# Kernel optimization log

Measured on AMD Instinct MI355X. Metric: run time of the kernel, lower is better.

Reference implementation:

```python
import jax, jax.numpy as jnp
import numpy as np

B, H, W, F, D = 8, 126, 126, 64, 32
ITERS, NIT = 3, 20
RHO, NU, DT, FRC = 1.0, 0.1, 0.1, 1.0
DX = 2.0 / (B + 1)
DY = 2.0 / (H + 1)
DX2, DY2 = DX * DX, DY * DY
DEN = 2.0 * (DX2 + DY2)


def _b_term(du_dx, dv_dy, du_dy, dv_dx):
    return RHO * ((du_dx + dv_dy) / DT - du_dx**2 - 2.0 * du_dy * dv_dx - dv_dy**2)


def build_b(u, v):
    b = jnp.zeros_like(u)
    # interior
    b = b.at[:, 1:-1, 1:-1].set(_b_term(
        (u[:, 1:-1, 2:] - u[:, 1:-1, :-2]) / (2 * DX),
        (v[:, 2:, 1:-1] - v[:, :-2, 1:-1]) / (2 * DY),
        (u[:, 2:, 1:-1] - u[:, :-2, 1:-1]) / (2 * DY),
        (v[:, 1:-1, 2:] - v[:, 1:-1, :-2]) / (2 * DX)))
    # periodic wrap, last column
    b = b.at[:, 1:-1, -1].set(_b_term(
        (u[:, 1:-1, 0] - u[:, 1:-1, -2]) / (2 * DX),
        (v[:, 2:, -1] - v[:, :-2, -1]) / (2 * DY),
        (u[:, 2:, -1] - u[:, :-2, -1]) / (2 * DY),
        (v[:, 1:-1, 0] - v[:, 1:-1, -2]) / (2 * DX)))
    # periodic wrap, first column
    b = b.at[:, 1:-1, 0].set(_b_term(
        (u[:, 1:-1, 1] - u[:, 1:-1, -1]) / (2 * DX),
        (v[:, 2:, 0] - v[:, :-2, 0]) / (2 * DY),
        (u[:, 2:, 0] - u[:, :-2, 0]) / (2 * DY),
        (v[:, 1:-1, 1] - v[:, 1:-1, -1]) / (2 * DX)))
    return b


def pressure_poisson(p, b):
    c = DX2 * DY2 / DEN

    def step(p, _):
        pn = p
        p = p.at[:, 1:-1, 1:-1].set(
            ((pn[:, 1:-1, 2:] + pn[:, 1:-1, :-2]) * DY2 + (pn[:, 2:, 1:-1] + pn[:, :-2, 1:-1]) * DX2) / DEN
            - c * b[:, 1:-1, 1:-1])
        p = p.at[:, 1:-1, -1].set(
            ((pn[:, 1:-1, 0] + pn[:, 1:-1, -2]) * DY2 + (pn[:, 2:, -1] + pn[:, :-2, -1]) * DX2) / DEN
            - c * b[:, 1:-1, -1])
        p = p.at[:, 1:-1, 0].set(
            ((pn[:, 1:-1, 1] + pn[:, 1:-1, -1]) * DY2 + (pn[:, 2:, 0] + pn[:, :-2, 0]) * DX2) / DEN
            - c * b[:, 1:-1, 0])
        # Neumann-style row boundaries (copy from updated p, as in torch code)
        p = p.at[:, -1].set(p[:, -2])
        p = p.at[:, 0].set(p[:, 1])
        return p, None

    p, _ = jax.lax.scan(step, p, None, length=NIT)
    return p


def velocity_step(u, v, p):
    un, vn = u, v
    uc = un[:, 1:-1, 1:-1]
    vc = vn[:, 1:-1, 1:-1]
    u_i = (uc - uc * DT / DX * (uc - un[:, 1:-1, :-2]) - vc * DT / DY * (uc - un[:, :-2, 1:-1])
           - DT / (2 * RHO * DX) * (p[:, 1:-1, 2:] - p[:, 1:-1, :-2])
           + NU * (DT / DX2 * (un[:, 1:-1, 2:] - 2 * uc + un[:, 1:-1, :-2])
                   + DT / DY2 * (un[:, 2:, 1:-1] - 2 * uc + un[:, :-2, 1:-1]))
           + FRC * DT)
    v_i = (vc - uc * DT / DX * (vc - vn[:, 1:-1, :-2]) - vc * DT / DY * (vc - vn[:, :-2, 1:-1])
           - DT / (2 * RHO * DY) * (p[:, 2:, 1:-1] - p[:, :-2, 1:-1])
           + NU * (DT / DX2 * (vn[:, 1:-1, 2:] - 2 * vc + vn[:, 1:-1, :-2])
                   + DT / DY2 * (vn[:, 2:, 1:-1] - 2 * vc + vn[:, :-2, 1:-1])))
    ue = un[:, 1:-1, -1]
    ve = vn[:, 1:-1, -1]
    u_e = (ue - ue * DT / DX * (ue - un[:, 1:-1, -2]) - ve * DT / DY * (ue - un[:, :-2, -1])
           - DT / (2 * RHO * DX) * (p[:, 1:-1, 0] - p[:, 1:-1, -2])
           + NU * (DT / DX2 * (un[:, 1:-1, 0] - 2 * ue + un[:, 1:-1, -2])
                   + DT / DY2 * (un[:, 2:, -1] - 2 * ue + un[:, :-2, -1]))
           + FRC * DT)
    v_e = (ve - ue * DT / DX * (ve - vn[:, 1:-1, -2]) - ve * DT / DY * (ve - vn[:, :-2, -1])
           - DT / (2 * RHO * DY) * (p[:, 2:, -1] - p[:, :-2, -1])
           + NU * (DT / DX2 * (vn[:, 1:-1, 0] - 2 * ve + vn[:, 1:-1, -2])
                   + DT / DY2 * (vn[:, 2:, -1] - 2 * ve + vn[:, :-2, -1])))
    u0c = un[:, 1:-1, 0]
    v0c = vn[:, 1:-1, 0]
    u_0 = (u0c - u0c * DT / DX * (u0c - un[:, 1:-1, -1]) - v0c * DT / DY * (u0c - un[:, :-2, 0])
           - DT / (2 * RHO * DX) * (p[:, 1:-1, 1] - p[:, 1:-1, -1])
           + NU * (DT / DX2 * (un[:, 1:-1, 1] - 2 * u0c + un[:, 1:-1, -1])
                   + DT / DY2 * (un[:, 2:, 0] - 2 * u0c + un[:, :-2, 0]))
           + FRC * DT)
    v_0 = (v0c - u0c * DT / DX * (v0c - vn[:, 1:-1, -1]) - v0c * DT / DY * (v0c - vn[:, :-2, 0])
           - DT / (2 * RHO * DY) * (p[:, 2:, 0] - p[:, :-2, 0])
           + NU * (DT / DX2 * (vn[:, 1:-1, 1] - 2 * v0c + vn[:, 1:-1, -1])
                   + DT / DY2 * (vn[:, 2:, 0] - 2 * v0c + vn[:, :-2, 0])))
    u = un.at[:, 1:-1, 1:-1].set(u_i).at[:, 1:-1, -1].set(u_e).at[:, 1:-1, 0].set(u_0)
    v = vn.at[:, 1:-1, 1:-1].set(v_i).at[:, 1:-1, -1].set(v_e).at[:, 1:-1, 0].set(v_0)
    u = u.at[:, 0].set(0.0).at[:, -1].set(0.0)
    v = v.at[:, 0].set(0.0).at[:, -1].set(0.0)
    return u, v


def setup_inputs() -> dict:
    key = jax.random.key(0)
    ks = jax.random.split(key, 5)
    x = jax.random.normal(ks[0], (B, H, W, F), jnp.float32) * 0.05
    u0 = jax.random.normal(ks[1], (B, H + 2, W + 2, D), jnp.float32) * 0.05
    v0 = jax.random.normal(ks[2], (B, H + 2, W + 2, D), jnp.float32) * 0.05
    w = jax.random.normal(ks[3], (D, F), jnp.float32) / np.float32(np.sqrt(F))
    b_lin = jax.random.normal(ks[4], (D,), jnp.float32) * 0.01
    return {"x": x, "u0": u0, "v0": v0, "w": w, "b_lin": b_lin}


def reference(x, u0, v0, w, b_lin):
    # pad spatial dims by 1 then linear preprocess: (B,H+2,W+2,F) -> (B,H+2,W+2,D)
    p = jnp.pad(x, ((0, 0), (1, 1), (1, 1), (0, 0)))
    p = jnp.einsum('bhwf,df->bhwd', p, w) + b_lin
    u, v = u0, v0
    for _ in range(ITERS):
        b = build_b(u, v)
        p = pressure_poisson(p, b)
        u, v = velocity_step(u, v, p)
    return p[:, -1, :, :]  # (B, W+2, D)
```

## Files before the change

kernel.cpp:

```cpp
#include <hip/hip_runtime.h>

#define NITER 20
#define OUTER 3

constexpr double DXd  = 2.0 / 9.0;
constexpr double DYd  = 2.0 / 127.0;
constexpr double DX2d = DXd * DXd;
constexpr double DY2d = DYd * DYd;
constexpr double DENd = 2.0 * (DX2d + DY2d);

constexpr float K1     = (float)(DY2d / DENd);
constexpr float K2     = (float)(DX2d / DENd);
constexpr float CC     = (float)(DX2d * DY2d / DENd);
constexpr float INV2DX = (float)(1.0 / (2.0 * DXd));
constexpr float INV2DY = (float)(1.0 / (2.0 * DYd));
constexpr float INVDT  = (float)(1.0 / 0.1);
constexpr float DTDX   = (float)(0.1 / DXd);
constexpr float DTDY   = (float)(0.1 / DYd);
constexpr float PGX    = (float)(0.1 / (2.0 * 1.0 * DXd));
constexpr float PGY    = (float)(0.1 / (2.0 * 1.0 * DYd));
constexpr float A1     = (float)(0.1 / DX2d);
constexpr float A2     = (float)(0.1 / DY2d);
constexpr float NUf    = 0.1f;
constexpr float FDT    = 0.1f;

__device__ __forceinline__ float bperm(int srcByte, float v) {
    return __int_as_float(__builtin_amdgcn_ds_bpermute(srcByte, __float_as_int(v)));
}

__global__ __launch_bounds__(256) void einsum_kernel(
    const float* __restrict__ x, const float* __restrict__ w,
    const float* __restrict__ bl, float* __restrict__ p0)
{
    int id = blockIdx.x * 256 + threadIdx.x;
    int c = id & 127, r = (id >> 7) & 127, b = id >> 14;
    float acc[32];
#pragma unroll
    for (int d = 0; d < 32; ++d) acc[d] = bl[d];
    if (r >= 1 && r <= 126 && c >= 1 && c <= 126) {
        const float* xp = x + (((size_t)(b * 126 + (r - 1))) * 126 + (c - 1)) * 64;
#pragma unroll
        for (int f = 0; f < 64; f += 4) {
            float4 xv = *(const float4*)(xp + f);
#pragma unroll
            for (int d = 0; d < 32; ++d) {
                acc[d] += xv.x * w[d * 64 + f] + xv.y * w[d * 64 + f + 1]
                        + xv.z * w[d * 64 + f + 2] + xv.w * w[d * 64 + f + 3];
            }
        }
    }
    float* op = p0 + ((size_t)b * 32) * 16384 + r * 128 + c;
#pragma unroll
    for (int d = 0; d < 32; ++d) op[(size_t)d * 16384] = acc[d];
}

__global__ __launch_bounds__(1024, 4) void sim_kernel(
    const float* __restrict__ u0, const float* __restrict__ v0,
    const float* __restrict__ p0ws, const float* __restrict__ x,
    const float* __restrict__ w, const float* __restrict__ bl,
    float* __restrict__ out, int use_ws)
{
    __shared__ float S[32][4][128];

    const int tid = threadIdx.x;
    const int tx = tid & 31, ty = tid >> 5;
    const int c0 = tx << 2, r0 = ty << 2;
    const int lane = tid & 63;
    const int srcL = (((lane & 32) | ((lane + 31) & 31)) << 2);
    const int srcR = (((lane & 32) | ((lane + 1) & 31)) << 2);
    const int bb = blockIdx.x & 7;
    const int d  = blockIdx.x >> 3;
    const int tyN = (ty > 0) ? ty - 1 : 0;
    const int tyS = (ty < 31) ? ty + 1 : 31;

    float pC[4][4], uC[4][4], vC[4][4], cb[4][4];

#pragma unroll
    for (int r = 0; r < 4; ++r) {
        const size_t base = ((size_t)((bb * 128 + (r0 + r)) * 128 + c0)) * 32 + d;
#pragma unroll
        for (int c = 0; c < 4; ++c) {
            uC[r][c] = u0[base + (size_t)c * 32];
            vC[r][c] = v0[base + (size_t)c * 32];
        }
    }

    if (use_ws) {
        const float* pp = p0ws + ((size_t)(bb * 32 + d)) * 16384;
#pragma unroll
        for (int r = 0; r < 4; ++r) {
            float4 t = *(const float4*)(pp + (r0 + r) * 128 + c0);
            pC[r][0] = t.x; pC[r][1] = t.y; pC[r][2] = t.z; pC[r][3] = t.w;
        }
    } else {
        const float blv = bl[d];
#pragma unroll
        for (int r = 0; r < 4; ++r) {
            const int gr = r0 + r;
#pragma unroll
            for (int c = 0; c < 4; ++c) {
                const int gc = c0 + c;
                float acc = blv;
                if (gr >= 1 && gr <= 126 && gc >= 1 && gc <= 126) {
                    const float* xp = x + (((size_t)(bb * 126 + (gr - 1))) * 126 + (gc - 1)) * 64;
                    for (int f = 0; f < 64; f += 4) {
                        float4 xv = *(const float4*)(xp + f);
                        acc += xv.x * w[d * 64 + f] + xv.y * w[d * 64 + f + 1]
                             + xv.z * w[d * 64 + f + 2] + xv.w * w[d * 64 + f + 3];
                    }
                }
                pC[r][c] = acc;
            }
        }
    }

    *(float4*)&S[ty][0][c0] = make_float4(uC[0][0], uC[0][1], uC[0][2], uC[0][3]);
    *(float4*)&S[ty][1][c0] = make_float4(uC[3][0], uC[3][1], uC[3][2], uC[3][3]);
    *(float4*)&S[ty][2][c0] = make_float4(vC[0][0], vC[0][1], vC[0][2], vC[0][3]);
    *(float4*)&S[ty][3][c0] = make_float4(vC[3][0], vC[3][1], vC[3][2], vC[3][3]);
    __syncthreads();

    for (int outer = 0; outer < OUTER; ++outer) {
        float4 uN4 = *(const float4*)&S[tyN][1][c0];
        float4 uS4 = *(const float4*)&S[tyS][0][c0];
        float4 vN4 = *(const float4*)&S[tyN][3][c0];
        float4 vS4 = *(const float4*)&S[tyS][2][c0];
        float uNh[4] = {uN4.x, uN4.y, uN4.z, uN4.w};
        float uSh[4] = {uS4.x, uS4.y, uS4.z, uS4.w};
        float vNh[4] = {vN4.x, vN4.y, vN4.z, vN4.w};
        float vSh[4] = {vS4.x, vS4.y, vS4.z, vS4.w};

#pragma unroll
        for (int r = 0; r < 4; ++r) {
            float uWh = bperm(srcL, uC[r][3]);
            float uEh = bperm(srcR, uC[r][0]);
            float vWh = bperm(srcL, vC[r][3]);
            float vEh = bperm(srcR, vC[r][0]);
#pragma unroll
            for (int c = 0; c < 4; ++c) {
                float uE = (c < 3) ? uC[r][c + 1] : uEh;
                float uW = (c > 0) ? uC[r][c - 1] : uWh;
                float vE = (c < 3) ? vC[r][c + 1] : vEh;
                float vW = (c > 0) ? vC[r][c - 1] : vWh;
                float uN = (r > 0) ? uC[r - 1][c] : uNh[c];
                float uS_ = (r < 3) ? uC[r + 1][c] : uSh[c];
                float vN = (r > 0) ? vC[r - 1][c] : vNh[c];
                float vS_ = (r < 3) ? vC[r + 1][c] : vSh[c];
                float dudx = (uE - uW) * INV2DX;
                float dvdy = (vS_ - vN) * INV2DY;
                float dudy = (uS_ - uN) * INV2DY;
                float dvdx = (vE - vW) * INV2DX;
                float bt = (dudx + dvdy) * INVDT - dudx * dudx
                         - 2.0f * dudy * dvdx - dvdy * dvdy;
                cb[r][c] = CC * bt;
            }
        }
        __syncthreads();
        *(float4*)&S[ty][0][c0] = make_float4(pC[0][0], pC[0][1], pC[0][2], pC[0][3]);
        *(float4*)&S[ty][1][c0] = make_float4(pC[3][0], pC[3][1], pC[3][2], pC[3][3]);
        __syncthreads();

        for (int it = 0; it < NITER; ++it) {
            const int rb = (it & 1) << 1;
            const int wb = rb ^ 2;
            float4 t4 = *(const float4*)&S[tyN][rb + 1][c0];
            float4 b4 = *(const float4*)&S[tyS][rb + 0][c0];
            float nrow[4] = {t4.x, t4.y, t4.z, t4.w};
            float shalo[4] = {b4.x, b4.y, b4.z, b4.w};
            float pWh[4], pEh[4];
#pragma unroll
            for (int r = 0; r < 4; ++r) {
                pWh[r] = bperm(srcL, pC[r][3]);
                pEh[r] = bperm(srcR, pC[r][0]);
            }
#pragma unroll
            for (int r = 0; r < 4; ++r) {
                float old0[4];
#pragma unroll
                for (int c = 0; c < 4; ++c) old0[c] = pC[r][c];
#pragma unroll
                for (int c = 0; c < 4; ++c) {
                    float E = (c < 3) ? old0[c + 1] : pEh[r];
                    float W = (c > 0) ? old0[c - 1] : pWh[r];
                    float N = nrow[c];
                    float Sv = (r < 3) ? pC[r + 1][c] : shalo[c];
                    pC[r][c] = (E + W) * K1 + (N + Sv) * K2 - cb[r][c];
                }
#pragma unroll
                for (int c = 0; c < 4; ++c) nrow[c] = old0[c];
            }
            if (ty == 0) {
#pragma unroll
                for (int c = 0; c < 4; ++c) pC[0][c] = pC[1][c];
            }
            if (ty == 31) {
#pragma unroll
                for (int c = 0; c < 4; ++c) pC[3][c] = pC[2][c];
            }
            *(float4*)&S[ty][wb][c0]     = make_float4(pC[0][0], pC[0][1], pC[0][2], pC[0][3]);
            *(float4*)&S[ty][wb + 1][c0] = make_float4(pC[3][0], pC[3][1], pC[3][2], pC[3][3]);
            __syncthreads();
        }

        if (outer < OUTER - 1) {
            float4 pt4 = *(const float4*)&S[tyN][1][c0];
            float4 pb4 = *(const float4*)&S[tyS][0][c0];
            float pNh[4] = {pt4.x, pt4.y, pt4.z, pt4.w};
            float pSh[4] = {pb4.x, pb4.y, pb4.z, pb4.w};

            float uNrow[4], vNrow[4];
#pragma unroll
            for (int c = 0; c < 4; ++c) { uNrow[c] = uNh[c]; vNrow[c] = vNh[c]; }
#pragma unroll
            for (int r = 0; r < 4; ++r) {
                float uold[4], vold[4];
#pragma unroll
                for (int c = 0; c < 4; ++c) { uold[c] = uC[r][c]; vold[c] = vC[r][c]; }
                float uWh = bperm(srcL, uold[3]);
                float uEh = bperm(srcR, uold[0]);
                float vWh = bperm(srcL, vold[3]);
                float vEh = bperm(srcR, vold[0]);
                float pWh = bperm(srcL, pC[r][3]);
                float pEh = bperm(srcR, pC[r][0]);
#pragma unroll
                for (int c = 0; c < 4; ++c) {
                    float uc = uold[c], vc = vold[c];
                    float uE = (c < 3) ? uold[c + 1] : uEh;
                    float uW = (c > 0) ? uold[c - 1] : uWh;
                    float vE = (c < 3) ? vold[c + 1] : vEh;
                    float vW = (c > 0) ? vold[c - 1] : vWh;
                    float uN = uNrow[c];
                    float uS_ = (r < 3) ? uC[r + 1][c] : uSh[c];
                    float vN = vNrow[c];
                    float vS_ = (r < 3) ? vC[r + 1][c] : vSh[c];
                    float pE = (c < 3) ? pC[r][c + 1] : pEh;
                    float pW = (c > 0) ? pC[r][c - 1] : pWh;
                    float pN = (r > 0) ? pC[r - 1][c] : pNh[c];
                    float pS = (r < 3) ? pC[r + 1][c] : pSh[c];

                    float unew = uc - uc * DTDX * (uc - uW) - vc * DTDY * (uc - uN)
                               - PGX * (pE - pW)
                               + NUf * (A1 * (uE - 2.0f * uc + uW) + A2 * (uS_ - 2.0f * uc + uN))
                               + FDT;
                    float vnew = vc - uc * DTDX * (vc - vW) - vc * DTDY * (vc - vN)
                               - PGY * (pS - pN)
                               + NUf * (A1 * (vE - 2.0f * vc + vW) + A2 * (vS_ - 2.0f * vc + vN));
                    uC[r][c] = unew;
                    vC[r][c] = vnew;
                }
#pragma unroll
                for (int c = 0; c < 4; ++c) { uNrow[c] = uold[c]; vNrow[c] = vold[c]; }
            }
            if (ty == 0) {
#pragma unroll
                for (int c = 0; c < 4; ++c) { uC[0][c] = 0.0f; vC[0][c] = 0.0f; }
            }
            if (ty == 31) {
#pragma unroll
                for (int c = 0; c < 4; ++c) { uC[3][c] = 0.0f; vC[3][c] = 0.0f; }
            }
            __syncthreads();
            *(float4*)&S[ty][0][c0] = make_float4(uC[0][0], uC[0][1], uC[0][2], uC[0][3]);
            *(float4*)&S[ty][1][c0] = make_float4(uC[3][0], uC[3][1], uC[3][2], uC[3][3]);
            *(float4*)&S[ty][2][c0] = make_float4(vC[0][0], vC[0][1], vC[0][2], vC[0][3]);
            *(float4*)&S[ty][3][c0] = make_float4(vC[3][0], vC[3][1], vC[3][2], vC[3][3]);
            __syncthreads();
        }
    }

    if (ty == 31) {
        float* op = out + ((size_t)bb * 128 + c0) * 32 + d;
        op[0]  = pC[3][0];
        op[32] = pC[3][1];
        op[64] = pC[3][2];
        op[96] = pC[3][3];
    }
}

extern "C" void kernel_launch(void* const* d_in, const int* in_sizes, int n_in,
                              void* d_out, int out_size, void* d_ws, size_t ws_size,
                              hipStream_t stream) {
    const float* x  = (const float*)d_in[0];
    const float* u0 = (const float*)d_in[1];
    const float* v0 = (const float*)d_in[2];
    const float* w  = (const float*)d_in[3];
    const float* bl = (const float*)d_in[4];
    float* out = (float*)d_out;
    float* p0  = (float*)d_ws;

    const size_t need = (size_t)8 * 32 * 128 * 128 * sizeof(float);
    const int use_ws = (ws_size >= need) ? 1 : 0;

    if (use_ws) {
        einsum_kernel<<<512, 256, 0, stream>>>(x, w, bl, p0);
    }
    sim_kernel<<<256, 1024, 0, stream>>>(u0, v0, p0, x, w, bl, out, use_ws);
}
```

Before: 287.7 us.

## Use 4x8 per-thread tiles, DPP row rotates, and separate double-buffered halo arrays

Halves the block to 512 threads and gives each thread a 4x8 tile, so the 16-lane row spans 128 columns. The ds_bpermute calls for horizontal halos become DPP row_ror moves, with a lane-identity test picking the rotation direction. Shared memory is split into double-buffered pressure halos and separate u/v halo arrays, which removes a barrier per phase. The cost is more registers per thread and fewer waves in flight, and correctness relies on the DPP rotation direction detection.

```diff
diff --git a/kernel.cpp b/kernel.cpp
--- a/kernel.cpp
+++ b/kernel.cpp
@@ -24,9 +24,10 @@
 constexpr float NUf    = 0.1f;
 constexpr float FDT    = 0.1f;
 
-__device__ __forceinline__ float bperm(int srcByte, float v) {
-    return __int_as_float(__builtin_amdgcn_ds_bpermute(srcByte, __float_as_int(v)));
-}
+#define ROR1(x)  __int_as_float(__builtin_amdgcn_mov_dpp(__float_as_int(x), 0x121, 0xF, 0xF, false))
+#define ROR15(x) __int_as_float(__builtin_amdgcn_mov_dpp(__float_as_int(x), 0x12F, 0xF, 0xF, false))
+#define FROM_LO(x) (selLower ? ROR1(x) : ROR15(x))
+#define FROM_HI(x) (selLower ? ROR15(x) : ROR1(x))
 
 __global__ __launch_bounds__(256) void einsum_kernel(
     const float* __restrict__ x, const float* __restrict__ w,
@@ -54,32 +55,35 @@
     for (int d = 0; d < 32; ++d) op[(size_t)d * 16384] = acc[d];
 }
 
-__global__ __launch_bounds__(1024, 4) void sim_kernel(
+__global__ __launch_bounds__(512, 2) void sim_kernel(
     const float* __restrict__ u0, const float* __restrict__ v0,
     const float* __restrict__ p0ws, const float* __restrict__ x,
     const float* __restrict__ w, const float* __restrict__ bl,
     float* __restrict__ out, int use_ws)
 {
-    __shared__ float S[32][4][128];
+    __shared__ float sP[2][32][2][128];
+    __shared__ float sU[32][2][128];
+    __shared__ float sV[32][2][128];
 
     const int tid = threadIdx.x;
-    const int tx = tid & 31, ty = tid >> 5;
-    const int c0 = tx << 2, r0 = ty << 2;
+    const int tx = tid & 15, ty = tid >> 4;
+    const int c0 = tx << 3, r0 = ty << 2;
     const int lane = tid & 63;
-    const int srcL = (((lane & 32) | ((lane + 31) & 31)) << 2);
-    const int srcR = (((lane & 32) | ((lane + 1) & 31)) << 2);
     const int bb = blockIdx.x & 7;
     const int d  = blockIdx.x >> 3;
     const int tyN = (ty > 0) ? ty - 1 : 0;
     const int tyS = (ty < 31) ? ty + 1 : 31;
 
-    float pC[4][4], uC[4][4], vC[4][4], cb[4][4];
+    const int pr = __builtin_amdgcn_mov_dpp(lane, 0x121, 0xF, 0xF, false);
+    const bool selLower = (pr == ((lane & 48) | ((lane + 15) & 15)));
+
+    float pC[4][8], uC[4][8], vC[4][8], cb[4][8];
 
 #pragma unroll
     for (int r = 0; r < 4; ++r) {
         const size_t base = ((size_t)((bb * 128 + (r0 + r)) * 128 + c0)) * 32 + d;
 #pragma unroll
-        for (int c = 0; c < 4; ++c) {
+        for (int c = 0; c < 8; ++c) {
             uC[r][c] = u0[base + (size_t)c * 32];
             vC[r][c] = v0[base + (size_t)c * 32];
         }
@@ -89,8 +93,10 @@
         const float* pp = p0ws + ((size_t)(bb * 32 + d)) * 16384;
 #pragma unroll
         for (int r = 0; r < 4; ++r) {
-            float4 t = *(const float4*)(pp + (r0 + r) * 128 + c0);
-            pC[r][0] = t.x; pC[r][1] = t.y; pC[r][2] = t.z; pC[r][3] = t.w;
+            float4 a = *(const float4*)(pp + (r0 + r) * 128 + c0);
+            float4 b = *(const float4*)(pp + (r0 + r) * 128 + c0 + 4);
+            pC[r][0] = a.x; pC[r][1] = a.y; pC[r][2] = a.z; pC[r][3] = a.w;
+            pC[r][4] = b.x; pC[r][5] = b.y; pC[r][6] = b.z; pC[r][7] = b.w;
         }
     } else {
         const float blv = bl[d];
@@ -98,7 +104,7 @@
         for (int r = 0; r < 4; ++r) {
             const int gr = r0 + r;
 #pragma unroll
-            for (int c = 0; c < 4; ++c) {
+            for (int c = 0; c < 8; ++c) {
                 const int gc = c0 + c;
                 float acc = blv;
                 if (gr >= 1 && gr <= 126 && gc >= 1 && gc <= 126) {
@@ -114,166 +120,191 @@
         }
     }
 
-    *(float4*)&S[ty][0][c0] = make_float4(uC[0][0], uC[0][1], uC[0][2], uC[0][3]);
-    *(float4*)&S[ty][1][c0] = make_float4(uC[3][0], uC[3][1], uC[3][2], uC[3][3]);
-    *(float4*)&S[ty][2][c0] = make_float4(vC[0][0], vC[0][1], vC[0][2], vC[0][3]);
-    *(float4*)&S[ty][3][c0] = make_float4(vC[3][0], vC[3][1], vC[3][2], vC[3][3]);
+    int s = 0;
+    *(float4*)&sP[0][ty][0][c0]     = make_float4(pC[0][0], pC[0][1], pC[0][2], pC[0][3]);
+    *(float4*)&sP[0][ty][0][c0 + 4] = make_float4(pC[0][4], pC[0][5], pC[0][6], pC[0][7]);
+    *(float4*)&sP[0][ty][1][c0]     = make_float4(pC[3][0], pC[3][1], pC[3][2], pC[3][3]);
+    *(float4*)&sP[0][ty][1][c0 + 4] = make_float4(pC[3][4], pC[3][5], pC[3][6], pC[3][7]);
+    *(float4*)&sU[ty][0][c0]        = make_float4(uC[0][0], uC[0][1], uC[0][2], uC[0][3]);
+    *(float4*)&sU[ty][0][c0 + 4]    = make_float4(uC[0][4], uC[0][5], uC[0][6], uC[0][7]);
+    *(float4*)&sU[ty][1][c0]        = make_float4(uC[3][0], uC[3][1], uC[3][2], uC[3][3]);
+    *(float4*)&sU[ty][1][c0 + 4]    = make_float4(uC[3][4], uC[3][5], uC[3][6], uC[3][7]);
+    *(float4*)&sV[ty][0][c0]        = make_float4(vC[0][0], vC[0][1], vC[0][2], vC[0][3]);
+    *(float4*)&sV[ty][0][c0 + 4]    = make_float4(vC[0][4], vC[0][5], vC[0][6], vC[0][7]);
+    *(float4*)&sV[ty][1][c0]        = make_float4(vC[3][0], vC[3][1], vC[3][2], vC[3][3]);
+    *(float4*)&sV[ty][1][c0 + 4]    = make_float4(vC[3][4], vC[3][5], vC[3][6], vC[3][7]);
     __syncthreads();
 
     for (int outer = 0; outer < OUTER; ++outer) {
-        float4 uN4 = *(const float4*)&S[tyN][1][c0];
-        float4 uS4 = *(const float4*)&S[tyS][0][c0];
-        float4 vN4 = *(const float4*)&S[tyN][3][c0];
-        float4 vS4 = *(const float4*)&S[tyS][2][c0];
-        float uNh[4] = {uN4.x, uN4.y, uN4.z, uN4.w};
-        float uSh[4] = {uS4.x, uS4.y, uS4.z, uS4.w};
-        float vNh[4] = {vN4.x, vN4.y, vN4.z, vN4.w};
-        float vSh[4] = {vS4.x, vS4.y, vS4.z, vS4.w};
-
-#pragma unroll
-        for (int r = 0; r < 4; ++r) {
-            float uWh = bperm(srcL, uC[r][3]);
-            float uEh = bperm(srcR, uC[r][0]);
-            float vWh = bperm(srcL, vC[r][3]);
-            float vEh = bperm(srcR, vC[r][0]);
-#pragma unroll
-            for (int c = 0; c < 4; ++c) {
-                float uE = (c < 3) ? uC[r][c + 1] : uEh;
-                float uW = (c > 0) ? uC[r][c - 1] : uWh;
-                float vE = (c < 3) ? vC[r][c + 1] : vEh;
-                float vW = (c > 0) ? vC[r][c - 1] : vWh;
-                float uN = (r > 0) ? uC[r - 1][c] : uNh[c];
-                float uS_ = (r < 3) ? uC[r + 1][c] : uSh[c];
-                float vN = (r > 0) ? vC[r - 1][c] : vNh[c];
-                float vS_ = (r < 3) ? vC[r + 1][c] : vSh[c];
-                float dudx = (uE - uW) * INV2DX;
-                float dvdy = (vS_ - vN) * INV2DY;
-                float dudy = (uS_ - uN) * INV2DY;
-                float dvdx = (vE - vW) * INV2DX;
-                float bt = (dudx + dvdy) * INVDT - dudx * dudx
-                         - 2.0f * dudy * dvdx - dvdy * dvdy;
-                cb[r][c] = CC * bt;
-            }
-        }
-        __syncthreads();
-        *(float4*)&S[ty][0][c0] = make_float4(pC[0][0], pC[0][1], pC[0][2], pC[0][3]);
-        *(float4*)&S[ty][1][c0] = make_float4(pC[3][0], pC[3][1], pC[3][2], pC[3][3]);
-        __syncthreads();
+        {
+            float uNh[8], uSh[8], vNh[8], vSh[8];
+            {
+                float4 a, b;
+                a = *(const float4*)&sU[tyN][1][c0]; b = *(const float4*)&sU[tyN][1][c0 + 4];
+                uNh[0]=a.x; uNh[1]=a.y; uNh[2]=a.z; uNh[3]=a.w; uNh[4]=b.x; uNh[5]=b.y; uNh[6]=b.z; uNh[7]=b.w;
+                a = *(const float4*)&sU[tyS][0][c0]; b = *(const float4*)&sU[tyS][0][c0 + 4];
+                uSh[0]=a.x; uSh[1]=a.y; uSh[2]=a.z; uSh[3]=a.w; uSh[4]=b.x; uSh[5]=b.y; uSh[6]=b.z; uSh[7]=b.w;
+                a = *(const float4*)&sV[tyN][1][c0]; b = *(const float4*)&sV[tyN][1][c0 + 4];
+                vNh[0]=a.x; vNh[1]=a.y; vNh[2]=a.z; vNh[3]=a.w; vNh[4]=b.x; vNh[5]=b.y; vNh[6]=b.z; vNh[7]=b.w;
+                a = *(const float4*)&sV[tyS][0][c0]; b = *(const float4*)&sV[tyS][0][c0 + 4];
+                vSh[0]=a.x; vSh[1]=a.y; vSh[2]=a.z; vSh[3]=a.w; vSh[4]=b.x; vSh[5]=b.y; vSh[6]=b.z; vSh[7]=b.w;
+            }
+#pragma unroll
+            for (int r = 0; r < 4; ++r) {
+                float uWh = FROM_LO(uC[r][7]);
+                float uEh = FROM_HI(uC[r][0]);
+                float vWh = FROM_LO(vC[r][7]);
+                float vEh = FROM_HI(vC[r][0]);
+#pragma unroll
+                for (int c = 0; c < 8; ++c) {
+                    float uE = (c < 7) ? uC[r][c + 1] : uEh;
+                    float uW = (c > 0) ? uC[r][c - 1] : uWh;
+                    float vE = (c < 7) ? vC[r][c + 1] : vEh;
+                    float vW = (c > 0) ? vC[r][c - 1] : vWh;
+                    float uN = (r > 0) ? uC[r - 1][c] : uNh[c];
+                    float uS = (r < 3) ? uC[r + 1][c] : uSh[c];
+                    float vN = (r > 0) ? vC[r - 1][c] : vNh[c];
+                    float vS = (r < 3) ? vC[r + 1][c] : vSh[c];
+                    float dudx = (uE - uW) * INV2DX;
+                    float dvdy = (vS - vN) * INV2DY;
+                    float dudy = (uS - uN) * INV2DY;
+                    float dvdx = (vE - vW) * INV2DX;
+                    float bt = (dudx + dvdy) * INVDT - dudx * dudx
+                             - 2.0f * dudy * dvdx - dvdy * dvdy;
+                    cb[r][c] = CC * bt;
+                }
+            }
+        }
 
         for (int it = 0; it < NITER; ++it) {
-            const int rb = (it & 1) << 1;
-            const int wb = rb ^ 2;
-            float4 t4 = *(const float4*)&S[tyN][rb + 1][c0];
-            float4 b4 = *(const float4*)&S[tyS][rb + 0][c0];
-            float nrow[4] = {t4.x, t4.y, t4.z, t4.w};
-            float shalo[4] = {b4.x, b4.y, b4.z, b4.w};
-            float pWh[4], pEh[4];
+            float nrow[8], shalo[8];
+            {
+                float4 a, b;
+                a = *(const float4*)&sP[s][tyN][1][c0]; b = *(const float4*)&sP[s][tyN][1][c0 + 4];
+                nrow[0]=a.x; nrow[1]=a.y; nrow[2]=a.z; nrow[3]=a.w; nrow[4]=b.x; nrow[5]=b.y; nrow[6]=b.z; nrow[7]=b.w;
+                a = *(const float4*)&sP[s][tyS][0][c0]; b = *(const float4*)&sP[s][tyS][0][c0 + 4];
+                shalo[0]=a.x; shalo[1]=a.y; shalo[2]=a.z; shalo[3]=a.w; shalo[4]=b.x; shalo[5]=b.y; shalo[6]=b.z; shalo[7]=b.w;
+            }
 #pragma unroll
             for (int r = 0; r < 4; ++r) {
-                pWh[r] = bperm(srcL, pC[r][3]);
-                pEh[r] = bperm(srcR, pC[r][0]);
-            }
+                float old0[8];
+#pragma unroll
+                for (int c = 0; c < 8; ++c) old0[c] = pC[r][c];
+                float pWh = FROM_LO(old0[7]);
+                float pEh = FROM_HI(old0[0]);
+#pragma unroll
+                for (int c = 0; c < 8; ++c) {
+                    float E = (c < 7) ? old0[c + 1] : pEh;
+                    float W = (c > 0) ? old0[c - 1] : pWh;
+                    float N = nrow[c];
+                    float S = (r < 3) ? pC[r + 1][c] : shalo[c];
+                    pC[r][c] = (E + W) * K1 + (N + S) * K2 - cb[r][c];
+                }
+#pragma unroll
+                for (int c = 0; c < 8; ++c) nrow[c] = old0[c];
+            }
+            if (ty == 0) {
+#pragma unroll
+                for (int c = 0; c < 8; ++c) pC[0][c] = pC[1][c];
+            }
+            if (ty == 31) {
+#pragma unroll
+                for (int c = 0; c < 8; ++c) pC[3][c] = pC[2][c];
+            }
+            *(float4*)&sP[s ^ 1][ty][0][c0]     = make_float4(pC[0][0], pC[0][1], pC[0][2], pC[0][3]);
+            *(float4*)&sP[s ^ 1][ty][0][c0 + 4] = make_float4(pC[0][4], pC[0][5], pC[0][6], pC[0][7]);
+            *(float4*)&sP[s ^ 1][ty][1][c0]     = make_float4(pC[3][0], pC[3][1], pC[3][2], pC[3][3]);
+            *(float4*)&sP[s ^ 1][ty][1][c0 + 4] = make_float4(pC[3][4], pC[3][5], pC[3][6], pC[3][7]);
+            __syncthreads();
+            s ^= 1;
+        }
+
+        if (outer < OUTER - 1) {
+            float uNh[8], uSh[8], vNh[8], vSh[8], pNh[8], pSh[8];
+            {
+                float4 a, b;
+                a = *(const float4*)&sU[tyN][1][c0]; b = *(const float4*)&sU[tyN][1][c0 + 4];
+                uNh[0]=a.x; uNh[1]=a.y; uNh[2]=a.z; uNh[3]=a.w; uNh[4]=b.x; uNh[5]=b.y; uNh[6]=b.z; uNh[7]=b.w;
+                a = *(const float4*)&sU[tyS][0][c0]; b = *(const float4*)&sU[tyS][0][c0 + 4];
+                uSh[0]=a.x; uSh[1]=a.y; uSh[2]=a.z; uSh[3]=a.w; uSh[4]=b.x; uSh[5]=b.y; uSh[6]=b.z; uSh[7]=b.w;
+                a = *(const float4*)&sV[tyN][1][c0]; b = *(const float4*)&sV[tyN][1][c0 + 4];
+                vNh[0]=a.x; vNh[1]=a.y; vNh[2]=a.z; vNh[3]=a.w; vNh[4]=b.x; vNh[5]=b.y; vNh[6]=b.z; vNh[7]=b.w;
+                a = *(const float4*)&sV[tyS][0][c0]; b = *(const float4*)&sV[tyS][0][c0 + 4];
+                vSh[0]=a.x; vSh[1]=a.y; vSh[2]=a.z; vSh[3]=a.w; vSh[4]=b.x; vSh[5]=b.y; vSh[6]=b.z; vSh[7]=b.w;
+                a = *(const float4*)&sP[s][tyN][1][c0]; b = *(const float4*)&sP[s][tyN][1][c0 + 4];
+                pNh[0]=a.x; pNh[1]=a.y; pNh[2]=a.z; pNh[3]=a.w; pNh[4]=b.x; pNh[5]=b.y; pNh[6]=b.z; pNh[7]=b.w;
+                a = *(const float4*)&sP[s][tyS][0][c0]; b = *(const float4*)&sP[s][tyS][0][c0 + 4];
+                pSh[0]=a.x; pSh[1]=a.y; pSh[2]=a.z; pSh[3]=a.w; pSh[4]=b.x; pSh[5]=b.y; pSh[6]=b.z; pSh[7]=b.w;
+            }
+            __syncthreads();
+
+            float uNrow[8], vNrow[8];
+#pragma unroll
+            for (int c = 0; c < 8; ++c) { uNrow[c] = uNh[c]; vNrow[c] = vNh[c]; }
 #pragma unroll
             for (int r = 0; r < 4; ++r) {
-                float old0[4];
-#pragma unroll
-                for (int c = 0; c < 4; ++c) old0[c] = pC[r][c];
-#pragma unroll
-                for (int c = 0; c < 4; ++c) {
-                    float E = (c < 3) ? old0[c + 1] : pEh[r];
-                    float W = (c > 0) ? old0[c - 1] : pWh[r];
-                    float N = nrow[c];
-                    float Sv = (r < 3) ? pC[r + 1][c] : shalo[c];
-                    pC[r][c] = (E + W) * K1 + (N + Sv) * K2 - cb[r][c];
-                }
-#pragma unroll
-                for (int c = 0; c < 4; ++c) nrow[c] = old0[c];
-            }
-            if (ty == 0) {
-#pragma unroll
-                for (int c = 0; c < 4; ++c) pC[0][c] = pC[1][c];
-            }
-            if (ty == 31) {
-#pragma unroll
-                for (int c = 0; c < 4; ++c) pC[3][c] = pC[2][c];
-            }
-            *(float4*)&S[ty][wb][c0]     = make_float4(pC[0][0], pC[0][1], pC[0][2], pC[0][3]);
-            *(float4*)&S[ty][wb + 1][c0] = make_float4(pC[3][0], pC[3][1], pC[3][2], pC[3][3]);
-            __syncthreads();
-        }
-
-        if (outer < OUTER - 1) {
-            float4 pt4 = *(const float4*)&S[tyN][1][c0];
-            float4 pb4 = *(const float4*)&S[tyS][0][c0];
-            float pNh[4] = {pt4.x, pt4.y, pt4.z, pt4.w};
-            float pSh[4] = {pb4.x, pb4.y, pb4.z, pb4.w};
-
-            float uNrow[4], vNrow[4];
-#pragma unroll
-            for (int c = 0; c < 4; ++c) { uNrow[c] = uNh[c]; vNrow[c] = vNh[c]; }
-#pragma unroll
-            for (int r = 0; r < 4; ++r) {
-                float uold[4], vold[4];
-#pragma unroll
-                for (int c = 0; c < 4; ++c) { uold[c] = uC[r][c]; vold[c] = vC[r][c]; }
-                float uWh = bperm(srcL, uold[3]);
-                float uEh = bperm(srcR, uold[0]);
-                float vWh = bperm(srcL, vold[3]);
-                float vEh = bperm(srcR, vold[0]);
-                float pWh = bperm(srcL, pC[r][3]);
-                float pEh = bperm(srcR, pC[r][0]);
-#pragma unroll
-                for (int c = 0; c < 4; ++c) {
+                float uold[8], vold[8];
+#pragma unroll
+                for (int c = 0; c < 8; ++c) { uold[c] = uC[r][c]; vold[c] = vC[r][c]; }
+                float uWh = FROM_LO(uold[7]);
+                float uEh = FROM_HI(uold[0]);
+                float vWh = FROM_LO(vold[7]);
+                float vEh = FROM_HI(vold[0]);
+                float pWh = FROM_LO(pC[r][7]);
+                float pEh = FROM_HI(pC[r][0]);
+#pragma unroll
+                for (int c = 0; c < 8; ++c) {
                     float uc = uold[c], vc = vold[c];
-                    float uE = (c < 3) ? uold[c + 1] : uEh;
+                    float uE = (c < 7) ? uold[c + 1] : uEh;
                     float uW = (c > 0) ? uold[c - 1] : uWh;
-                    float vE = (c < 3) ? vold[c + 1] : vEh;
+                    float vE = (c < 7) ? vold[c + 1] : vEh;
                     float vW = (c > 0) ? vold[c - 1] : vWh;
                     float uN = uNrow[c];
-                    float uS_ = (r < 3) ? uC[r + 1][c] : uSh[c];
+                    float uS = (r < 3) ? uC[r + 1][c] : uSh[c];
                     float vN = vNrow[c];
-                    float vS_ = (r < 3) ? vC[r + 1][c] : vSh[c];
-                    float pE = (c < 3) ? pC[r][c + 1] : pEh;
+                    float vS = (r < 3) ? vC[r + 1][c] : vSh[c];
+                    float pE = (c < 7) ? pC[r][c + 1] : pEh;
                     float pW = (c > 0) ? pC[r][c - 1] : pWh;
                     float pN = (r > 0) ? pC[r - 1][c] : pNh[c];
                     float pS = (r < 3) ? pC[r + 1][c] : pSh[c];
 
                     float unew = uc - uc * DTDX * (uc - uW) - vc * DTDY * (uc - uN)
                                - PGX * (pE - pW)
-                               + NUf * (A1 * (uE - 2.0f * uc + uW) + A2 * (uS_ - 2.0f * uc + uN))
+                               + NUf * (A1 * (uE - 2.0f * uc + uW) + A2 * (uS - 2.0f * uc + uN))
                                + FDT;
                     float vnew = vc - uc * DTDX * (vc - vW) - vc * DTDY * (vc - vN)
                                - PGY * (pS - pN)
-                               + NUf * (A1 * (vE - 2.0f * vc + vW) + A2 * (vS_ - 2.0f * vc + vN));
+                               + NUf * (A1 * (vE - 2.0f * vc + vW) + A2 * (vS - 2.0f * vc + vN));
                     uC[r][c] = unew;
                     vC[r][c] = vnew;
                 }
 #pragma unroll
-                for (int c = 0; c < 4; ++c) { uNrow[c] = uold[c]; vNrow[c] = vold[c]; }
+                for (int c = 0; c < 8; ++c) { uNrow[c] = uold[c]; vNrow[c] = vold[c]; }
             }
             if (ty == 0) {
 #pragma unroll
-                for (int c = 0; c < 4; ++c) { uC[0][c] = 0.0f; vC[0][c] = 0.0f; }
+                for (int c = 0; c < 8; ++c) { uC[0][c] = 0.0f; vC[0][c] = 0.0f; }
             }
             if (ty == 31) {
 #pragma unroll
-                for (int c = 0; c < 4; ++c) { uC[3][c] = 0.0f; vC[3][c] = 0.0f; }
-            }
-            __syncthreads();
-            *(float4*)&S[ty][0][c0] = make_float4(uC[0][0], uC[0][1], uC[0][2], uC[0][3]);
-            *(float4*)&S[ty][1][c0] = make_float4(uC[3][0], uC[3][1], uC[3][2], uC[3][3]);
-            *(float4*)&S[ty][2][c0] = make_float4(vC[0][0], vC[0][1], vC[0][2], vC[0][3]);
-            *(float4*)&S[ty][3][c0] = make_float4(vC[3][0], vC[3][1], vC[3][2], vC[3][3]);
+                for (int c = 0; c < 8; ++c) { uC[3][c] = 0.0f; vC[3][c] = 0.0f; }
+            }
+            *(float4*)&sU[ty][0][c0]     = make_float4(uC[0][0], uC[0][1], uC[0][2], uC[0][3]);
+            *(float4*)&sU[ty][0][c0 + 4] = make_float4(uC[0][4], uC[0][5], uC[0][6], uC[0][7]);
+            *(float4*)&sU[ty][1][c0]     = make_float4(uC[3][0], uC[3][1], uC[3][2], uC[3][3]);
+            *(float4*)&sU[ty][1][c0 + 4] = make_float4(uC[3][4], uC[3][5], uC[3][6], uC[3][7]);
+            *(float4*)&sV[ty][0][c0]     = make_float4(vC[0][0], vC[0][1], vC[0][2], vC[0][3]);
+            *(float4*)&sV[ty][0][c0 + 4] = make_float4(vC[0][4], vC[0][5], vC[0][6], vC[0][7]);
+            *(float4*)&sV[ty][1][c0]     = make_float4(vC[3][0], vC[3][1], vC[3][2], vC[3][3]);
+            *(float4*)&sV[ty][1][c0 + 4] = make_float4(vC[3][4], vC[3][5], vC[3][6], vC[3][7]);
             __syncthreads();
         }
     }
 
     if (ty == 31) {
         float* op = out + ((size_t)bb * 128 + c0) * 32 + d;
-        op[0]  = pC[3][0];
-        op[32] = pC[3][1];
-        op[64] = pC[3][2];
-        op[96] = pC[3][3];
+#pragma unroll
+        for (int c = 0; c < 8; ++c) op[(size_t)c * 32] = pC[3][c];
     }
 }
 
@@ -294,5 +325,5 @@
     if (use_ws) {
         einsum_kernel<<<512, 256, 0, stream>>>(x, w, bl, p0);
     }
-    sim_kernel<<<256, 1024, 0, stream>>>(u0, v0, p0, x, w, bl, out, use_ws);
+    sim_kernel<<<256, 512, 0, stream>>>(u0, v0, p0, x, w, bl, out, use_ws);
 }
```

Measured after the change: 282.2 us. No clear change (-1.9%).
